# Performance work log

Hardware: AMD Instinct MI355X
Metric: run time of the kernel (lower is better)

The kernel has to match this reference:

```python
import jax, jax.numpy as jnp
import numpy as np
import math

D_MODEL = 1024
NUM_HEADS = 16
THETA = 10000.0


def _rope(x, pos, theta):
    # x: (B, S, H, d_k), pos: (B, S) int32/64
    d_k = x.shape[-1]
    half = d_k // 2
    inv_freq = theta ** (-jnp.arange(half, dtype=jnp.float32) * 2.0 / d_k)  # (half,)
    ang = pos.astype(jnp.float32)[..., None] * inv_freq  # (B, S, half)
    cos = jnp.cos(ang)[..., None, :]  # (B, S, 1, half) broadcast over heads
    sin = jnp.sin(ang)[..., None, :]
    x1 = x[..., 0::2]  # even dims
    x2 = x[..., 1::2]  # odd dims
    out_even = x1 * cos - x2 * sin
    out_odd = x1 * sin + x2 * cos
    # re-interleave pairs
    return jnp.stack([out_even, out_odd], axis=-1).reshape(x.shape)


def setup_inputs() -> dict:
    key = jax.random.key(0)
    k0, k1, k2, k3, k4 = jax.random.split(key, 5)
    B, S, D = 4, 2048, D_MODEL
    std = math.sqrt(2.0 / (D + D))
    x = jax.random.normal(k0, (B, S, D), dtype=jnp.float32)
    wq = jax.random.normal(k1, (D, D), dtype=jnp.float32) * std
    wk = jax.random.normal(k2, (D, D), dtype=jnp.float32) * std
    wv = jax.random.normal(k3, (D, D), dtype=jnp.float32) * std
    wo = jax.random.normal(k4, (D, D), dtype=jnp.float32) * std
    return {"x": x, "wq": wq, "wk": wk, "wv": wv, "wo": wo}


def reference(x, wq, wk, wv, wo):
    B, S, D = x.shape
    H = NUM_HEADS
    d_k = D // H
    # torch Linear: y = x @ W.T
    q = (x @ wq.T).reshape(B, S, H, d_k)
    k = (x @ wk.T).reshape(B, S, H, d_k)
    v = (x @ wv.T).reshape(B, S, H, d_k)
    pos = jnp.broadcast_to(jnp.arange(S), (B, S))
    q = _rope(q, pos, THETA)
    k = _rope(k, pos, THETA)
    # (B, H, S, d_k)
    q = q.transpose(0, 2, 1, 3)
    k = k.transpose(0, 2, 1, 3)
    v = v.transpose(0, 2, 1, 3)
    scores = jnp.einsum("bhqd,bhkd->bhqk", q, k) / jnp.sqrt(jnp.float32(d_k))
    causal = jnp.tril(jnp.ones((S, S), dtype=bool))  # True = keep
    scores = jnp.where(causal, scores, -jnp.inf)
    attn = jax.nn.softmax(scores, axis=-1)
    out = jnp.einsum("bhqk,bhkd->bhqd", attn, v)
    out = out.transpose(0, 2, 1, 3).reshape(B, S, D)
    return out @ wo.T
```

## Files before the change

kernel.cpp:

```cpp
#include <hip/hip_runtime.h>

#define DEV __device__ __forceinline__

typedef float f32x4 __attribute__((ext_vector_type(4)));
typedef float f32x16 __attribute__((ext_vector_type(16)));
typedef __bf16 bf16x8 __attribute__((ext_vector_type(8)));
typedef unsigned u32x4 __attribute__((ext_vector_type(4)));
typedef unsigned short u16x8 __attribute__((ext_vector_type(8)));

static constexpr int BB = 4, SS = 2048, DD = 1024, HH = 16;
static constexpr int MM = BB * SS;
static constexpr float LOG2_THETA_OVER_HALF = 0.4152410118609203f;
static constexpr float SCL2 = 0.18033688011112042f;

DEV unsigned short f2b(float f) {
    unsigned u = __float_as_uint(f);
    unsigned r = (u + 0x7fffu + ((u >> 16) & 1u)) >> 16;
    return (unsigned short)r;
}
DEV float b2f(unsigned short h) { return __uint_as_float(((unsigned)h) << 16); }

DEV void gload16(const void* g, void* l) {
    __builtin_amdgcn_global_load_lds((const __attribute__((address_space(1))) void*)g,
                                     (__attribute__((address_space(3))) void*)l, 16, 0, 0);
}

DEV unsigned cvtpk(float lo, float hi) {
    unsigned r;
    asm("v_cvt_pk_bf16_f32 %0, %1, %2" : "=v"(r) : "v"(lo), "v"(hi));
    return r;
}

#define PH_BAR do { __builtin_amdgcn_sched_barrier(0); __builtin_amdgcn_s_barrier(); __builtin_amdgcn_sched_barrier(0); } while (0)

__global__ void k_f2b(const float* __restrict__ src, unsigned short* __restrict__ dst, int n) {
    int i = (blockIdx.x * blockDim.x + threadIdx.x) * 4;
    if (i >= n) return;
    float4 v = *reinterpret_cast<const float4*>(src + i);
    ushort4 o;
    o.x = f2b(v.x); o.y = f2b(v.y); o.z = f2b(v.z); o.w = f2b(v.w);
    *reinterpret_cast<ushort4*>(dst + i) = o;
}

__global__ void k_f2b4(const float* __restrict__ s0, const float* __restrict__ s1,
                       const float* __restrict__ s2, const float* __restrict__ s3,
                       unsigned short* __restrict__ dst) {
    int bid = blockIdx.x;
    int t = bid >> 10;
    const float* src = (t == 0) ? s0 : (t == 1) ? s1 : (t == 2) ? s2 : s3;
    int i = ((bid & 1023) * 256 + threadIdx.x) * 4;
    float4 v = *reinterpret_cast<const float4*>(src + i);
    ushort4 o;
    o.x = f2b(v.x); o.y = f2b(v.y); o.z = f2b(v.z); o.w = f2b(v.w);
    *reinterpret_cast<ushort4*>(dst + (size_t)t * DD * DD + i) = o;
}

template <int OUTF32>
__global__ __launch_bounds__(512, 2) void k_gemm8n(const unsigned short* __restrict__ A,
                                                   const unsigned short* __restrict__ Bw,
                                                   void* __restrict__ Cp, int ldc) {
    __shared__ __align__(16) unsigned short LdsA[4][128 * 64];
    __shared__ __align__(16) unsigned short LdsB[4][128 * 64];
    const int tid = threadIdx.x, lane = tid & 63, wid = tid >> 6;
    const int wm = wid >> 1, wn = wid & 1;
    const int fr = lane & 15, l4 = lane >> 4, sw = fr & 7;
    const int m0 = blockIdx.y * 256, n0 = blockIdx.x * 128;

    const int r0 = tid >> 3;
    const int cg = (tid & 7) ^ (r0 & 7);
    const unsigned short* aS = A  + (size_t)(m0 + r0) * 1024 + (cg << 3);
    const unsigned short* bS = Bw + (size_t)(n0 + r0) * 1024 + (cg << 3);
    unsigned short* dA = &LdsA[0][0];
    unsigned short* dB = &LdsB[0][0];
    const int dOf = wid * 512;

    f32x4 acc[4][4] = {};

#define STGA(t, h) do {                                                     \
        unsigned short* d_ = dA + (((2 * (t) + (h)) & 3) * 8192) + dOf;     \
        const unsigned short* s_ = aS + (size_t)(t) * 64 + (size_t)(h) * 131072; \
        gload16(s_, d_); gload16(s_ + 65536, d_ + 4096);                    \
    } while (0)
#define STGB(t) do {                                                        \
        unsigned short* d_ = dB + (((t) & 3) * 8192) + dOf;                 \
        const unsigned short* s_ = bS + (size_t)(t) * 64;                   \
        gload16(s_, d_); gload16(s_ + 65536, d_ + 4096);                    \
    } while (0)

    STGB(0);
    STGA(0, 0); STGA(0, 1);
    STGB(1);

    bf16x8 aF[2][2], bL[2][2], bH[2][2];

    for (int T = 0; T < 16; ++T) {
        if (T < 15) { asm volatile("s_waitcnt vmcnt(2)" ::: "memory"); }
        else        { asm volatile("s_waitcnt vmcnt(0)" ::: "memory"); }
        PH_BAR;

        const unsigned short* As_ = &LdsA[(2 * T + (wm >> 1)) & 3][0];
        const unsigned short* Bs_ = &LdsB[T & 3][0];
        const int aro = (wm & 1) * 64;
        const int bro = wn * 64;

#pragma unroll
        for (int m = 0; m < 2; ++m)
#pragma unroll
            for (int kk = 0; kk < 2; ++kk)
                aF[m][kk] = *(const bf16x8*)&As_[(aro + m * 16 + fr) * 64 + ((((kk << 2) | l4) ^ sw) << 3)];
#pragma unroll
        for (int n = 0; n < 2; ++n)
#pragma unroll
            for (int kk = 0; kk < 2; ++kk)
                bL[n][kk] = *(const bf16x8*)&Bs_[(bro + n * 16 + fr) * 64 + ((((kk << 2) | l4) ^ sw) << 3)];
        if (T + 1 < 16) STGA(T + 1, 0);
        __builtin_amdgcn_s_setprio(1);
#pragma unroll
        for (int m = 0; m < 2; ++m)
#pragma unroll
            for (int n = 0; n < 2; ++n)
#pragma unroll
                for (int kk = 0; kk < 2; ++kk)
                    acc[m][n] = __builtin_amdgcn_mfma_f32_16x16x32_bf16(aF[m][kk], bL[n][kk], acc[m][n], 0, 0, 0);
        __builtin_amdgcn_s_setprio(0);
        PH_BAR;

#pragma unroll
        for (int n = 0; n < 2; ++n)
#pragma unroll
            for (int kk = 0; kk < 2; ++kk)
                bH[n][kk] = *(const bf16x8*)&Bs_[(bro + (n + 2) * 16 + fr) * 64 + ((((kk << 2) | l4) ^ sw) << 3)];
        if (T + 1 < 16) STGA(T + 1, 1);
        __builtin_amdgcn_s_setprio(1);
#pragma unroll
        for (int m = 0; m < 2; ++m)
#pragma unroll
            for (int n = 0; n < 2; ++n)
#pragma unroll
                for (int kk = 0; kk < 2; ++kk)
                    acc[m][n + 2] = __builtin_amdgcn_mfma_f32_16x16x32_bf16(aF[m][kk], bH[n][kk], acc[m][n + 2], 0, 0, 0);
        __builtin_amdgcn_s_setprio(0);
        PH_BAR;

#pragma unroll
        for (int m = 0; m < 2; ++m)
#pragma unroll
            for (int kk = 0; kk < 2; ++kk)
                aF[m][kk] = *(const bf16x8*)&As_[(aro + (m + 2) * 16 + fr) * 64 + ((((kk << 2) | l4) ^ sw) << 3)];
        if (T + 2 < 16) STGB(T + 2);
        __builtin_amdgcn_s_setprio(1);
#pragma unroll
        for (int m = 0; m < 2; ++m)
#pragma unroll
            for (int n = 0; n < 2; ++n)
#pragma unroll
                for (int kk = 0; kk < 2; ++kk)
                    acc[m + 2][n + 2] = __builtin_amdgcn_mfma_f32_16x16x32_bf16(aF[m][kk], bH[n][kk], acc[m + 2][n + 2], 0, 0, 0);
#pragma unroll
        for (int m = 0; m < 2; ++m)
#pragma unroll
            for (int n = 0; n < 2; ++n)
#pragma unroll
                for (int kk = 0; kk < 2; ++kk)
                    acc[m + 2][n] = __builtin_amdgcn_mfma_f32_16x16x32_bf16(aF[m][kk], bL[n][kk], acc[m + 2][n], 0, 0, 0);
        __builtin_amdgcn_s_setprio(0);
    }
#undef STGA
#undef STGB

    const int rb = l4 * 4;
#pragma unroll
    for (int m = 0; m < 4; ++m)
#pragma unroll
        for (int n = 0; n < 4; ++n)
#pragma unroll
            for (int r = 0; r < 4; ++r) {
                int row = m0 + wm * 64 + m * 16 + rb + r;
                int col = n0 + wn * 64 + n * 16 + fr;
                if (OUTF32) ((float*)Cp)[(size_t)row * ldc + col] = acc[m][n][r];
                else        ((unsigned short*)Cp)[(size_t)row * ldc + col] = f2b(acc[m][n][r]);
            }
}

__global__ void k_ropeQK(unsigned short* __restrict__ T) {
    int g = blockIdx.x * blockDim.x + threadIdx.x;
    int m = g >> 9, p = g & 511;
    int i = p & 31;
    int s = m & (SS - 1);
    int col = ((p >> 5) << 6) + (i << 1);
    float inv = exp2f(-(float)i * LOG2_THETA_OVER_HALF);
    float ang = (float)s * inv;
    float sn, cs;
    sincosf(ang, &sn, &cs);
    unsigned short* q2 = T + (size_t)m * 3072 + col;
    unsigned short* k2 = q2 + 1024;
    float q1 = b2f(q2[0]), q2v = b2f(q2[1]);
    float k1 = b2f(k2[0]), k2v = b2f(k2[1]);
    q2[0] = f2b((q1 * cs - q2v * sn) * SCL2);
    q2[1] = f2b((q1 * sn + q2v * cs) * SCL2);
    k2[0] = f2b(k1 * cs - k2v * sn);
    k2[1] = f2b(k1 * sn + k2v * cs);
}

__global__ __launch_bounds__(256) void k_vt(const unsigned short* __restrict__ V,
                                            unsigned short* __restrict__ Vt) {
    __shared__ unsigned short T[64 * 65];
    const int tid = threadIdx.x;
    const int s0 = blockIdx.x * 64, bh = blockIdx.y;
    const int b = bh >> 4, h = bh & 15;
    const int r = tid >> 3, c8 = (tid & 7) * 8;
#pragma unroll
    for (int p = 0; p < 2; p++) {
        int row = p * 32 + r;
        u16x8 v = *(const u16x8*)&V[(size_t)(b * SS + s0 + row) * 3072 + h * 64 + c8];
#pragma unroll
        for (int j = 0; j < 8; j++) T[(c8 + j) * 65 + row] = v[j];
    }
    __syncthreads();
#pragma unroll
    for (int p = 0; p < 2; p++) {
        int d = p * 32 + r;
        u16x8 o;
#pragma unroll
        for (int j = 0; j < 8; j++) o[j] = T[d * 65 + c8 + j];
        *(u16x8*)&Vt[((size_t)bh * 64 + d) * 2048 + s0 + c8] = o;
    }
}

DEV void packp(const f32x16& s, bf16x8* pf) {
#pragma unroll
    for (int g = 0; g < 2; g++) {
        unsigned w0 = cvtpk(s[8 * g + 0], s[8 * g + 1]);
        unsigned w1 = cvtpk(s[8 * g + 2], s[8 * g + 3]);
        unsigned w2 = cvtpk(s[8 * g + 4], s[8 * g + 5]);
        unsigned w3 = cvtpk(s[8 * g + 6], s[8 * g + 7]);
        asm("v_permlane32_swap_b32 %0, %1" : "+v"(w0), "+v"(w2));
        asm("v_permlane32_swap_b32 %0, %1" : "+v"(w1), "+v"(w3));
        u32x4 pd;
        pd[0] = w0; pd[1] = w1; pd[2] = w2; pd[3] = w3;
        pf[g] = __builtin_bit_cast(bf16x8, pd);
    }
}

DEV float sum16(const f32x16& s) {
    return (((s[0] + s[1]) + (s[2] + s[3])) + ((s[4] + s[5]) + (s[6] + s[7]))) +
           (((s[8] + s[9]) + (s[10] + s[11])) + (((s[12] + s[13]) + (s[14] + s[15]))));
}

__global__ __launch_bounds__(512, 4) void k_attn(const unsigned short* __restrict__ QKV,
                                                 const unsigned short* __restrict__ Vt,
                                                 unsigned short* __restrict__ O) {
    __shared__ __align__(16) unsigned short Kbuf[2][64 * 64];
    __shared__ __align__(16) unsigned short Vbuf[2][64 * 64];
    const int tid = threadIdx.x, lane = tid & 63, wid = tid >> 6;
    const int l31 = lane & 31, hi = lane >> 5;
    const int bh = blockIdx.x, b = bh >> 4, h = bh & 15;
    const int qt = gridDim.y - 1 - blockIdx.y;
    const int q0 = qt * 256;
    const int wq0 = q0 + wid * 32;
    const int tdw = wq0 >> 6;
    const int nk = (q0 + 256) >> 6;

    const int srow = tid >> 3, sc = tid & 7;
    const unsigned short* ksrc = QKV + 1024 + ((size_t)(b * SS) + srow) * 3072 + h * 64 + ((sc ^ (srow & 7)) << 3);
    const unsigned short* vsrc = Vt + ((size_t)(bh * 64) + srow) * 2048 + ((sc ^ (srow & 7)) << 3);

    const unsigned short* qp = QKV + (size_t)(b * SS + wq0 + l31) * 3072 + h * 64;
    bf16x8 qf[4];
#pragma unroll
    for (int dt = 0; dt < 4; dt++) qf[dt] = *(const bf16x8*)(qp + dt * 16 + hi * 8);

    f32x16 oacc0 = {}, oacc1 = {};
    float lrow = 0.f;
    const int swz = l31 & 7;

    gload16(ksrc, (unsigned short*)Kbuf[0] + wid * 512);
    gload16(vsrc, (unsigned short*)Vbuf[0] + wid * 512);

    for (int t = 0; t < nk; t++) {
        __syncthreads();
        if (t + 1 < nk) {
            gload16(ksrc + (size_t)(t + 1) * 64 * 3072, (unsigned short*)Kbuf[(t + 1) & 1] + wid * 512);
            gload16(vsrc + (t + 1) * 64,                (unsigned short*)Vbuf[(t + 1) & 1] + wid * 512);
        }
        if (t > tdw) continue;
        const unsigned short* Ks = Kbuf[t & 1];
        const unsigned short* Vs = Vbuf[t & 1];

        if (t < tdw) {
            f32x16 s0 = {}, s1 = {};
            __builtin_amdgcn_s_setprio(1);
#pragma unroll
            for (int dt = 0; dt < 4; dt++) {
                bf16x8 kf = *(const bf16x8*)&Ks[l31 * 64 + (((dt * 2 + hi) ^ swz) << 3)];
                s0 = __builtin_amdgcn_mfma_f32_32x32x16_bf16(kf, qf[dt], s0, 0, 0, 0);
            }
#pragma unroll
            for (int dt = 0; dt < 4; dt++) {
                bf16x8 kf = *(const bf16x8*)&Ks[(32 + l31) * 64 + (((dt * 2 + hi) ^ swz) << 3)];
                s1 = __builtin_amdgcn_mfma_f32_32x32x16_bf16(kf, qf[dt], s1, 0, 0, 0);
            }
            __builtin_amdgcn_s_setprio(0);
#pragma unroll
            for (int r = 0; r < 16; r++) {
                s0[r] = __builtin_amdgcn_exp2f(s0[r]);
                s1[r] = __builtin_amdgcn_exp2f(s1[r]);
            }
            lrow += sum16(s0) + sum16(s1);
            bf16x8 pA[2], pB[2];
            packp(s0, pA);
            packp(s1, pB);
            __builtin_amdgcn_s_setprio(1);
#pragma unroll
            for (int g = 0; g < 2; g++) {
                bf16x8 vf0 = *(const bf16x8*)&Vs[l31 * 64 + (((g * 2 + hi) ^ swz) << 3)];
                oacc0 = __builtin_amdgcn_mfma_f32_32x32x16_bf16(vf0, pA[g], oacc0, 0, 0, 0);
                bf16x8 vf1 = *(const bf16x8*)&Vs[(32 + l31) * 64 + (((g * 2 + hi) ^ swz) << 3)];
                oacc1 = __builtin_amdgcn_mfma_f32_32x32x16_bf16(vf1, pA[g], oacc1, 0, 0, 0);
            }
#pragma unroll
            for (int g = 0; g < 2; g++) {
                bf16x8 vf0 = *(const bf16x8*)&Vs[l31 * 64 + (((4 + g * 2 + hi) ^ swz) << 3)];
                oacc0 = __builtin_amdgcn_mfma_f32_32x32x16_bf16(vf0, pB[g], oacc0, 0, 0, 0);
                bf16x8 vf1 = *(const bf16x8*)&Vs[(32 + l31) * 64 + (((4 + g * 2 + hi) ^ swz) << 3)];
                oacc1 = __builtin_amdgcn_mfma_f32_32x32x16_bf16(vf1, pB[g], oacc1, 0, 0, 0);
            }
            __builtin_amdgcn_s_setprio(0);
        } else {
#pragma unroll
            for (int kt2 = 0; kt2 < 2; kt2++) {
                const int kb = t * 64 + kt2 * 32;
                if (kb > wq0) break;

                f32x16 sacc = {};
                __builtin_amdgcn_s_setprio(1);
#pragma unroll
                for (int dt = 0; dt < 4; dt++) {
                    bf16x8 kf = *(const bf16x8*)&Ks[(kt2 * 32 + l31) * 64 + (((dt * 2 + hi) ^ swz) << 3)];
                    sacc = __builtin_amdgcn_mfma_f32_32x32x16_bf16(kf, qf[dt], sacc, 0, 0, 0);
                }
                __builtin_amdgcn_s_setprio(0);

                if (kb == wq0) {
#pragma unroll
                    for (int r = 0; r < 16; r++) {
                        int kr = (r & 3) + 8 * (r >> 2) + 4 * hi;
                        sacc[r] = (kr > l31) ? -1e30f : sacc[r];
                    }
                }

#pragma unroll
                for (int r = 0; r < 16; r++) sacc[r] = __builtin_amdgcn_exp2f(sacc[r]);
                lrow += sum16(sacc);

                bf16x8 pf[2];
                packp(sacc, pf);

                __builtin_amdgcn_s_setprio(1);
#pragma unroll
                for (int g = 0; g < 2; g++) {
                    bf16x8 vf0 = *(const bf16x8*)&Vs[l31 * 64 + (((kt2 * 4 + g * 2 + hi) ^ swz) << 3)];
                    oacc0 = __builtin_amdgcn_mfma_f32_32x32x16_bf16(vf0, pf[g], oacc0, 0, 0, 0);
                    bf16x8 vf1 = *(const bf16x8*)&Vs[(32 + l31) * 64 + (((kt2 * 4 + g * 2 + hi) ^ swz) << 3)];
                    oacc1 = __builtin_amdgcn_mfma_f32_32x32x16_bf16(vf1, pf[g], oacc1, 0, 0, 0);
                }
                __builtin_amdgcn_s_setprio(0);
            }
        }
    }

    float lsum = lrow + __shfl_xor(lrow, 32);
    float linv = 1.0f / lsum;
    unsigned short* op = O + (size_t)(b * SS + wq0 + l31) * 1024 + h * 64 + hi * 4;
#pragma unroll
    for (int g = 0; g < 4; g++) {
        uint2 u;
        u.x = cvtpk(oacc0[4 * g + 0] * linv, oacc0[4 * g + 1] * linv);
        u.y = cvtpk(oacc0[4 * g + 2] * linv, oacc0[4 * g + 3] * linv);
        *(uint2*)&op[g * 8] = u;
        uint2 v;
        v.x = cvtpk(oacc1[4 * g + 0] * linv, oacc1[4 * g + 1] * linv);
        v.y = cvtpk(oacc1[4 * g + 2] * linv, oacc1[4 * g + 3] * linv);
        *(uint2*)&op[32 + g * 8] = v;
    }
}

extern "C" void kernel_launch(void* const* d_in, const int* in_sizes, int n_in,
                              void* d_out, int out_size, void* d_ws, size_t ws_size,
                              hipStream_t stream) {
    const float* x  = (const float*)d_in[0];
    const float* wq = (const float*)d_in[1];
    const float* wk = (const float*)d_in[2];
    const float* wv = (const float*)d_in[3];
    const float* wo = (const float*)d_in[4];
    float* out = (float*)d_out;

    unsigned short* xb    = (unsigned short*)d_ws;
    unsigned short* wqkvb = xb + (size_t)MM * DD;
    unsigned short* wob   = wqkvb + (size_t)3 * DD * DD;
    unsigned short* QKV   = wob + (size_t)DD * DD;
    unsigned short* Ob    = QKV + (size_t)MM * 3 * DD;
    unsigned short* Vtb   = xb;

    k_f2b<<<MM * DD / 4 / 256, 256, 0, stream>>>(x, xb, MM * DD);
    k_f2b4<<<4096, 256, 0, stream>>>(wq, wk, wv, wo, wqkvb);

    dim3 gq(3 * DD / 128, MM / 256);
    k_gemm8n<0><<<gq, 512, 0, stream>>>(xb, wqkvb, (void*)QKV, 3 * DD);

    int npair = MM * 512;
    k_ropeQK<<<npair / 256, 256, 0, stream>>>(QKV);

    dim3 gv(SS / 64, BB * HH);
    k_vt<<<gv, 256, 0, stream>>>(QKV + 2 * DD, Vtb);

    dim3 ga(BB * HH, SS / 256);
    k_attn<<<ga, 512, 0, stream>>>(QKV, Vtb, Ob);

    dim3 go(DD / 128, MM / 256);
    k_gemm8n<1><<<go, 512, 0, stream>>>(Ob, wob, (void*)out, DD);
}
```

Before: 189.8 us.

## Use 256x256 tile GEMM with 8-phase schedule for QKV projection

Adds a new bf16 GEMM kernel with 256x256 output tiles (8 waves arranged 2x4, each computing 128x64) and a four-phase interleaving of LDS fragment loads, global-to-LDS prefetch and MFMA with priority raising. The QKV projection now launches this kernel instead of the 256x128 variant, halving grid width. The aim is higher arithmetic intensity per byte loaded and better overlap of loads with MFMA. The trade-offs are larger accumulator register use and fewer blocks (12x32), which can hurt occupancy or wave balance across CUs.

```diff
diff --git a/kernel.cpp b/kernel.cpp
--- a/kernel.cpp
+++ b/kernel.cpp
@@ -53,6 +53,137 @@
     ushort4 o;
     o.x = f2b(v.x); o.y = f2b(v.y); o.z = f2b(v.z); o.w = f2b(v.w);
     *reinterpret_cast<ushort4*>(dst + (size_t)t * DD * DD + i) = o;
+}
+
+__global__ __launch_bounds__(512, 2) void k_gemm8(const unsigned short* __restrict__ A,
+                                                  const unsigned short* __restrict__ Bw,
+                                                  unsigned short* __restrict__ C, int ldc) {
+    __shared__ __align__(16) unsigned short LdsA[4][128 * 64];
+    __shared__ __align__(16) unsigned short LdsB[4][128 * 64];
+    const int tid = threadIdx.x, lane = tid & 63, wid = tid >> 6;
+    const int wm = wid >> 2, wn = wid & 3;
+    const int fr = lane & 15, l4 = lane >> 4, sw = fr & 7;
+    const int m0 = blockIdx.y * 256, n0 = blockIdx.x * 256;
+
+    const int r0 = tid >> 3;
+    const int cg = (tid & 7) ^ (r0 & 7);
+    const unsigned short* aS = A  + (size_t)(m0 + r0) * 1024 + (cg << 3);
+    const unsigned short* bS = Bw + (size_t)(n0 + r0) * 1024 + (cg << 3);
+    unsigned short* dA = &LdsA[0][0];
+    unsigned short* dB = &LdsB[0][0];
+    const int dOf = wid * 512;
+
+    f32x4 acc[8][4] = {};
+
+#define STG(src, base, slot) do {                         \
+        unsigned short* d_ = (base) + (slot) * 8192 + dOf;\
+        gload16((src), d_);                               \
+        gload16((src) + 64 * 1024, d_ + 4096);            \
+    } while (0)
+
+#pragma unroll
+    for (int T = 0; T < 2; ++T) {
+        STG(bS + T * 64,          dB, (2 * T) & 3);
+        STG(bS + T * 64 + 131072, dB, (2 * T + 1) & 3);
+        STG(aS + T * 64,          dA, (2 * T) & 3);
+        STG(aS + T * 64 + 131072, dA, (2 * T + 1) & 3);
+    }
+
+    bf16x8 aF[4][2], bL[2][2], bH[2][2];
+
+    for (int T = 0; T < 16; ++T) {
+        if (T < 15) { asm volatile("s_waitcnt vmcnt(8)" ::: "memory"); }
+        else        { asm volatile("s_waitcnt vmcnt(0)" ::: "memory"); }
+        PH_BAR;
+
+        const unsigned short* As_ = &LdsA[(2 * T + wm) & 3][0];
+        const unsigned short* Bs_ = &LdsB[(2 * T + (wn >> 1)) & 3][0];
+        const int bro = (wn & 1) * 64;
+
+#pragma unroll
+        for (int m = 0; m < 4; ++m)
+#pragma unroll
+            for (int kk = 0; kk < 2; ++kk)
+                aF[m][kk] = *(const bf16x8*)&As_[(m * 16 + fr) * 64 + ((((kk << 2) | l4) ^ sw) << 3)];
+#pragma unroll
+        for (int n = 0; n < 2; ++n)
+#pragma unroll
+            for (int kk = 0; kk < 2; ++kk)
+                bL[n][kk] = *(const bf16x8*)&Bs_[(bro + n * 16 + fr) * 64 + ((((kk << 2) | l4) ^ sw) << 3)];
+        __builtin_amdgcn_s_setprio(1);
+#pragma unroll
+        for (int m = 0; m < 4; ++m)
+#pragma unroll
+            for (int n = 0; n < 2; ++n)
+#pragma unroll
+                for (int kk = 0; kk < 2; ++kk)
+                    acc[m][n] = __builtin_amdgcn_mfma_f32_16x16x32_bf16(aF[m][kk], bL[n][kk], acc[m][n], 0, 0, 0);
+        __builtin_amdgcn_s_setprio(0);
+        PH_BAR;
+
+#pragma unroll
+        for (int n = 0; n < 2; ++n)
+#pragma unroll
+            for (int kk = 0; kk < 2; ++kk)
+                bH[n][kk] = *(const bf16x8*)&Bs_[(bro + (n + 2) * 16 + fr) * 64 + ((((kk << 2) | l4) ^ sw) << 3)];
+        __builtin_amdgcn_s_setprio(1);
+#pragma unroll
+        for (int m = 0; m < 4; ++m)
+#pragma unroll
+            for (int n = 0; n < 2; ++n)
+#pragma unroll
+                for (int kk = 0; kk < 2; ++kk)
+                    acc[m][n + 2] = __builtin_amdgcn_mfma_f32_16x16x32_bf16(aF[m][kk], bH[n][kk], acc[m][n + 2], 0, 0, 0);
+        __builtin_amdgcn_s_setprio(0);
+        PH_BAR;
+
+#pragma unroll
+        for (int m = 0; m < 4; ++m)
+#pragma unroll
+            for (int kk = 0; kk < 2; ++kk)
+                aF[m][kk] = *(const bf16x8*)&As_[((m + 4) * 16 + fr) * 64 + ((((kk << 2) | l4) ^ sw) << 3)];
+        if (T + 2 < 16) {
+            STG(bS + (T + 2) * 64,          dB, (2 * T) & 3);
+            STG(bS + (T + 2) * 64 + 131072, dB, (2 * T + 1) & 3);
+        }
+        __builtin_amdgcn_s_setprio(1);
+#pragma unroll
+        for (int m = 0; m < 4; ++m)
+#pragma unroll
+            for (int n = 0; n < 2; ++n)
+#pragma unroll
+                for (int kk = 0; kk < 2; ++kk)
+                    acc[m + 4][n + 2] = __builtin_amdgcn_mfma_f32_16x16x32_bf16(aF[m][kk], bH[n][kk], acc[m + 4][n + 2], 0, 0, 0);
+        __builtin_amdgcn_s_setprio(0);
+        PH_BAR;
+
+        if (T + 2 < 16) {
+            STG(aS + (T + 2) * 64,          dA, (2 * T) & 3);
+            STG(aS + (T + 2) * 64 + 131072, dA, (2 * T + 1) & 3);
+        }
+        __builtin_amdgcn_s_setprio(1);
+#pragma unroll
+        for (int m = 0; m < 4; ++m)
+#pragma unroll
+            for (int n = 0; n < 2; ++n)
+#pragma unroll
+                for (int kk = 0; kk < 2; ++kk)
+                    acc[m + 4][n] = __builtin_amdgcn_mfma_f32_16x16x32_bf16(aF[m][kk], bL[n][kk], acc[m + 4][n], 0, 0, 0);
+        __builtin_amdgcn_s_setprio(0);
+    }
+#undef STG
+
+    const int rb = l4 * 4;
+#pragma unroll
+    for (int m = 0; m < 8; ++m)
+#pragma unroll
+        for (int n = 0; n < 4; ++n)
+#pragma unroll
+            for (int r = 0; r < 4; ++r) {
+                int row = m0 + wm * 128 + m * 16 + rb + r;
+                int col = n0 + wn * 64 + n * 16 + fr;
+                C[(size_t)row * ldc + col] = f2b(acc[m][n][r]);
+            }
 }
 
 template <int OUTF32>
@@ -405,8 +536,8 @@
     k_f2b<<<MM * DD / 4 / 256, 256, 0, stream>>>(x, xb, MM * DD);
     k_f2b4<<<4096, 256, 0, stream>>>(wq, wk, wv, wo, wqkvb);
 
-    dim3 gq(3 * DD / 128, MM / 256);
-    k_gemm8n<0><<<gq, 512, 0, stream>>>(xb, wqkvb, (void*)QKV, 3 * DD);
+    dim3 gq(3 * DD / 256, MM / 256);
+    k_gemm8<<<gq, 512, 0, stream>>>(xb, wqkvb, QKV, 3 * DD);
 
     int npair = MM * 512;
     k_ropeQK<<<npair / 256, 256, 0, stream>>>(QKV);
```

New measurement: 182.3 us. 1.04x faster.
